# Performance work log

Measured on AMD Instinct MI355X. Metric: run time of the kernel, lower is better.

Reference implementation:

```python
import jax, jax.numpy as jnp
import numpy as np

IN_FEATURES = 2048
OUT_FEATURES = 2048
BLOCK_SIZE = 16
F_BLOCKS = (OUT_FEATURES + BLOCK_SIZE - 1) // BLOCK_SIZE  # 128
G_BLOCKS = (IN_FEATURES + BLOCK_SIZE - 1) // BLOCK_SIZE   # 128
BATCH = 4096


def setup_inputs() -> dict:
    key = jax.random.key(0)
    k1, k2, k3 = jax.random.split(key, 3)
    x = jax.random.normal(k1, (BATCH, IN_FEATURES), dtype=jnp.float32)
    # Xavier-uniform-ish scale for index vectors viewed as (f*g, block_size)
    limit = np.sqrt(6.0 / (F_BLOCKS * G_BLOCKS + BLOCK_SIZE)).astype(np.float32)
    index_vectors = jax.random.uniform(
        k2, (F_BLOCKS, G_BLOCKS, BLOCK_SIZE), dtype=jnp.float32,
        minval=-limit, maxval=limit)
    b = jax.random.normal(k3, (OUT_FEATURES,), dtype=jnp.float32) * 0.02
    return {"x": x, "index_vectors": index_vectors, "b": b}


def reference(x, index_vectors, b):
    batch = x.shape[0]
    padded_in = G_BLOCKS * BLOCK_SIZE
    padded_out = F_BLOCKS * BLOCK_SIZE
    if x.shape[1] < padded_in:
        x = jnp.pad(x, ((0, 0), (0, padded_in - x.shape[1])))
    x_blocks = x.reshape(batch, G_BLOCKS, BLOCK_SIZE)            # (B, g, b)
    # Batched FFT over all blocks at once (replaces the f*g python loop)
    fft_p = jnp.fft.fft(index_vectors, axis=-1)                  # (f, g, b) complex
    fft_x = jnp.fft.fft(x_blocks, axis=-1)                       # (B, g, b) complex
    # sum_j IFFT(P_ij * X_j) == IFFT(sum_j P_ij * X_j) by linearity of IFFT
    out_fft = jnp.einsum('fgb,Bgb->Bfb', fft_p, fft_x)           # (B, f, b) complex
    out_blocks = jnp.fft.ifft(out_fft, axis=-1).real             # (B, f, b)
    out = out_blocks.reshape(batch, padded_out)
    if padded_out > OUT_FEATURES:
        out = out[:, :OUT_FEATURES]
    return out + b
```

## Files before the change

kernel.cpp:

```cpp
#include <hip/hip_runtime.h>
#include <hip/hip_bf16.h>


#define M_DIM 4096
#define N_DIM 2048
#define K_DIM 2048
#define BK 64
#define NT (K_DIM / BK)
#define BUFSZ 49152

typedef __attribute__((ext_vector_type(8))) short bf16x8;
typedef __attribute__((ext_vector_type(4))) float f32x4;

typedef const __attribute__((address_space(1))) void gvoid_t;
typedef __attribute__((address_space(3))) void lvoid_t;

#define FENCE asm volatile("" ::: "memory")
#define BAR()  do { FENCE; __builtin_amdgcn_s_barrier(); FENCE; } while (0)
#define GLD(src, dst) __builtin_amdgcn_global_load_lds((gvoid_t*)(src), (lvoid_t*)(dst), 16, 0, 0)

#define STAGE_A(dst, src) (GLD((src) + 0 * 64 * K_DIM, (dst) + 0),     \
                           GLD((src) + 1 * 64 * K_DIM, (dst) + 8192),  \
                           GLD((src) + 2 * 64 * K_DIM, (dst) + 16384), \
                           GLD((src) + 3 * 64 * K_DIM, (dst) + 24576))
#define STAGE_B(dst, src) (GLD((src) + 0 * 64 * K_DIM, (dst) + 0),     \
                           GLD((src) + 1 * 64 * K_DIM, (dst) + 8192))

__device__ __forceinline__ unsigned int f2bf(float f) {
  unsigned int u = __float_as_uint(f);
  return (u + 0x7fffu + ((u >> 16) & 1u)) >> 16;
}

__global__ __launch_bounds__(256) void prep_kernel(const float* __restrict__ x,
                                                   const float* __restrict__ iv,
                                                   unsigned short* __restrict__ xb,
                                                   unsigned short* __restrict__ W) {
  int b = blockIdx.x;
  if (b < (M_DIM * K_DIM / 8) / 256) {
    int idx = b * 256 + threadIdx.x;
    const float4* x4 = (const float4*)x;
    float4 a = x4[idx * 2 + 0];
    float4 c = x4[idx * 2 + 1];
    uint4 o;
    o.x = f2bf(a.x) | (f2bf(a.y) << 16);
    o.y = f2bf(a.z) | (f2bf(a.w) << 16);
    o.z = f2bf(c.x) | (f2bf(c.y) << 16);
    o.w = f2bf(c.z) | (f2bf(c.w) << 16);
    ((uint4*)xb)[idx] = o;
  } else {
    int idx = (b - (M_DIM * K_DIM / 8) / 256) * 256 + threadIdx.x;
    int o  = idx >> 8;
    int i0 = (idx & 255) * 8;
    int f = o >> 4, t = o & 15;
    int g = i0 >> 4, u0 = i0 & 15;
    const float* row = iv + (f * 128 + g) * 16;
    unsigned int p[4];
#pragma unroll
    for (int j = 0; j < 4; ++j) {
      unsigned int lo = f2bf(row[(t - (u0 + 2 * j + 0)) & 15]);
      unsigned int hi = f2bf(row[(t - (u0 + 2 * j + 1)) & 15]);
      p[j] = lo | (hi << 16);
    }
    ((uint4*)W)[idx] = make_uint4(p[0], p[1], p[2], p[3]);
  }
}

__global__ __launch_bounds__(512, 2) void gemm_bias_kernel(const unsigned short* __restrict__ A,
                                                           const unsigned short* __restrict__ B,
                                                           const float* __restrict__ bias,
                                                           float* __restrict__ C) {
  __shared__ char lds[3 * BUFSZ];

  const int tid = threadIdx.x;
  const int l   = tid & 63;
  const int w   = tid >> 6;
  const int wm  = w >> 1;
  const int wn  = w & 1;

  const int orig = blockIdx.x;
  const int swz  = (orig & 7) * 32 + (orig >> 3);
  const int bm   = swz >> 4;
  const int bn   = swz & 15;

  f32x4 acc[4][4] = {};

  const int srow  = w * 8 + (l >> 3);
  const int sslot = (l & 7) ^ ((l >> 3) & 7);
  const unsigned short* Asrc0 = A + (size_t)(bm * 256 + srow) * K_DIM + sslot * 8;
  const unsigned short* Bsrc0 = B + (size_t)(bn * 128 + srow) * K_DIM + sslot * 8;

  const int fr = l & 15;
  const int rxor = (l & 7) << 4;
  const int aRow0 = (wm * 64 + fr) * 128;
  const int bRow0 = (wn * 64 + fr) * 128;
  const int swzcol0 = (0 * 64 + (l >> 4) * 16) ^ rxor;
  const int swzcol1 = (1 * 64 + (l >> 4) * 16) ^ rxor;

  bf16x8 fa[4], fb[4];

#define LDA(BUF, SWZ)                                                   \
  do {                                                                  \
    const char* Ab_ = lds + (BUF) * BUFSZ;                              \
    const char* Bb_ = Ab_ + 32768;                                      \
    _Pragma("unroll")                                                   \
    for (int m = 0; m < 4; ++m)                                         \
      fa[m] = *(const bf16x8*)(Ab_ + aRow0 + m * 2048 + (SWZ));         \
    _Pragma("unroll")                                                   \
    for (int n = 0; n < 4; ++n)                                         \
      fb[n] = *(const bf16x8*)(Bb_ + bRow0 + n * 2048 + (SWZ));         \
  } while (0)

#define MFMA_CLUSTER()                                                  \
  do {                                                                  \
    asm volatile("s_waitcnt lgkmcnt(0)" ::: "memory");                  \
    __builtin_amdgcn_sched_barrier(0);                                  \
    __builtin_amdgcn_s_setprio(1);                                      \
    _Pragma("unroll")                                                   \
    for (int m = 0; m < 4; ++m)                                         \
      _Pragma("unroll")                                                 \
      for (int n = 0; n < 4; ++n)                                       \
        acc[m][n] = __builtin_amdgcn_mfma_f32_16x16x32_bf16(fa[m], fb[n], acc[m][n], 0, 0, 0); \
    __builtin_amdgcn_s_setprio(0);                                      \
    __builtin_amdgcn_sched_barrier(0);                                  \
  } while (0)

#define PHASE(BUF, SWZ, STAGE_STMT, VM_STMT)                            \
  do {                                                                  \
    LDA(BUF, SWZ);                                                      \
    STAGE_STMT;                                                         \
    VM_STMT;                                                            \
    BAR();                                                              \
    MFMA_CLUSTER();                                                     \
    BAR();                                                              \
  } while (0)

#define VM6 asm volatile("s_waitcnt vmcnt(6)" ::: "memory")
#define VM0 asm volatile("s_waitcnt vmcnt(0)" ::: "memory")
#define NOSTAGE (void)0
#define NOVM (void)0

#define BODY(T, CUR, STG)                                               \
  do {                                                                  \
    PHASE(CUR, swzcol0, STAGE_A(lds + (STG) * BUFSZ + w * 1024, Asrc0 + ((T) + 2) * BK), NOVM); \
    PHASE(CUR, swzcol1, STAGE_B(lds + (STG) * BUFSZ + 32768 + w * 1024, Bsrc0 + ((T) + 2) * BK), VM6); \
  } while (0)

  STAGE_A(lds + 0 * BUFSZ + w * 1024, Asrc0 + 0 * BK);
  STAGE_B(lds + 0 * BUFSZ + 32768 + w * 1024, Bsrc0 + 0 * BK);
  STAGE_A(lds + 1 * BUFSZ + w * 1024, Asrc0 + 1 * BK);
  STAGE_B(lds + 1 * BUFSZ + 32768 + w * 1024, Bsrc0 + 1 * BK);
  asm volatile("s_waitcnt vmcnt(6)" ::: "memory");
  BAR();

  for (int t = 0; t < NT - 2; t += 3) {
    BODY(t + 0, 0, 2);
    BODY(t + 1, 1, 0);
    BODY(t + 2, 2, 1);
  }

  PHASE(0, swzcol0, NOSTAGE, NOVM);
  PHASE(0, swzcol1, NOSTAGE, VM0);
  LDA(1, swzcol0);
  MFMA_CLUSTER();
  LDA(1, swzcol1);
  MFMA_CLUSTER();

  const int row0 = bm * 256 + wm * 64 + (l >> 4) * 4;
  const int col0 = bn * 128 + wn * 64 + (l & 15);
#pragma unroll
  for (int n = 0; n < 4; ++n) {
    float bv = bias[col0 + n * 16];
#pragma unroll
    for (int m = 0; m < 4; ++m) {
#pragma unroll
      for (int j = 0; j < 4; ++j) {
        C[(size_t)(row0 + m * 16 + j) * N_DIM + (col0 + n * 16)] = acc[m][n][j] + bv;
      }
    }
  }
#undef BODY
#undef PHASE
#undef MFMA_CLUSTER
#undef LDA
#undef VM6
#undef VM0
#undef NOSTAGE
#undef NOVM
}

__global__ __launch_bounds__(256) void fallback_kernel(const float* __restrict__ x,
                                                       const float* __restrict__ iv,
                                                       const float* __restrict__ b,
                                                       float* __restrict__ out) {
  int idx = blockIdx.x * 256 + threadIdx.x;
  int Bn = idx >> 11, o = idx & 2047;
  int f = o >> 4, t = o & 15;
  const float* xr = x + (size_t)Bn * 2048;
  float acc = 0.f;
  for (int g = 0; g < 128; ++g) {
    const float* pr = iv + (f * 128 + g) * 16;
    const float* xg = xr + g * 16;
#pragma unroll
    for (int s = 0; s < 16; ++s) acc += pr[s] * xg[(t - s) & 15];
  }
  out[idx] = acc + b[o];
}

extern "C" void kernel_launch(void* const* d_in, const int* in_sizes, int n_in,
                              void* d_out, int out_size, void* d_ws, size_t ws_size,
                              hipStream_t stream) {
  const float* x    = (const float*)d_in[0];
  const float* iv   = (const float*)d_in[1];
  const float* bias = (const float*)d_in[2];
  float* out = (float*)d_out;

  const size_t xb_bytes = (size_t)M_DIM * K_DIM * 2;
  const size_t w_bytes  = (size_t)N_DIM * K_DIM * 2;
  if (ws_size < xb_bytes + w_bytes) {
    fallback_kernel<<<(M_DIM * N_DIM) / 256, 256, 0, stream>>>(x, iv, bias, out);
    return;
  }

  unsigned short* xb = (unsigned short*)d_ws;
  unsigned short* W  = xb + (size_t)M_DIM * K_DIM;

  const int cvt_blocks = (M_DIM * K_DIM / 8) / 256;
  const int bw_blocks  = (N_DIM * K_DIM / 8) / 256;
  prep_kernel<<<cvt_blocks + bw_blocks, 256, 0, stream>>>(x, iv, xb, W);

  gemm_bias_kernel<<<(M_DIM / 256) * (N_DIM / 128), 512, 0, stream>>>(xb, W, bias, out);
}
```

Before: 56.81 us.

## Shrink GEMM tile to 128x128 with 256 threads and double buffering

Changes the GEMM block tile from 256x128 with 8 waves to 128x128 with 4 waves, doubling the grid to 512 blocks. The three-stage LDS ring with split A/B phases becomes a two-buffer scheme: each step issues the next tile's A and B loads together, runs both MFMA clusters with a single barrier, then waits on vmcnt(0). The aim is less LDS per block, more blocks per CU and fewer barriers. The cost is lower operand reuse per block, more global traffic, and less prefetch depth, since each iteration now waits for all loads to finish.

```diff
diff --git a/kernel.cpp b/kernel.cpp
--- a/kernel.cpp
+++ b/kernel.cpp
@@ -7,7 +7,7 @@
 #define K_DIM 2048
 #define BK 64
 #define NT (K_DIM / BK)
-#define BUFSZ 49152
+#define BUFSZ 32768
 
 typedef __attribute__((ext_vector_type(8))) short bf16x8;
 typedef __attribute__((ext_vector_type(4))) float f32x4;
@@ -18,13 +18,6 @@
 #define FENCE asm volatile("" ::: "memory")
 #define BAR()  do { FENCE; __builtin_amdgcn_s_barrier(); FENCE; } while (0)
 #define GLD(src, dst) __builtin_amdgcn_global_load_lds((gvoid_t*)(src), (lvoid_t*)(dst), 16, 0, 0)
-
-#define STAGE_A(dst, src) (GLD((src) + 0 * 64 * K_DIM, (dst) + 0),     \
-                           GLD((src) + 1 * 64 * K_DIM, (dst) + 8192),  \
-                           GLD((src) + 2 * 64 * K_DIM, (dst) + 16384), \
-                           GLD((src) + 3 * 64 * K_DIM, (dst) + 24576))
-#define STAGE_B(dst, src) (GLD((src) + 0 * 64 * K_DIM, (dst) + 0),     \
-                           GLD((src) + 1 * 64 * K_DIM, (dst) + 8192))
 
 __device__ __forceinline__ unsigned int f2bf(float f) {
   unsigned int u = __float_as_uint(f);
@@ -65,11 +58,11 @@
   }
 }
 
-__global__ __launch_bounds__(512, 2) void gemm_bias_kernel(const unsigned short* __restrict__ A,
+__global__ __launch_bounds__(256, 2) void gemm_bias_kernel(const unsigned short* __restrict__ A,
                                                            const unsigned short* __restrict__ B,
                                                            const float* __restrict__ bias,
                                                            float* __restrict__ C) {
-  __shared__ char lds[3 * BUFSZ];
+  __shared__ char lds[2 * BUFSZ];
 
   const int tid = threadIdx.x;
   const int l   = tid & 63;
@@ -78,7 +71,7 @@
   const int wn  = w & 1;
 
   const int orig = blockIdx.x;
-  const int swz  = (orig & 7) * 32 + (orig >> 3);
+  const int swz  = (orig & 7) * 64 + (orig >> 3);
   const int bm   = swz >> 4;
   const int bn   = swz & 15;
 
@@ -86,7 +79,7 @@
 
   const int srow  = w * 8 + (l >> 3);
   const int sslot = (l & 7) ^ ((l >> 3) & 7);
-  const unsigned short* Asrc0 = A + (size_t)(bm * 256 + srow) * K_DIM + sslot * 8;
+  const unsigned short* Asrc0 = A + (size_t)(bm * 128 + srow) * K_DIM + sslot * 8;
   const unsigned short* Bsrc0 = B + (size_t)(bn * 128 + srow) * K_DIM + sslot * 8;
 
   const int fr = l & 15;
@@ -98,10 +91,26 @@
 
   bf16x8 fa[4], fb[4];
 
+#define STAGE_AB(BUFC, T)                                               \
+  do {                                                                  \
+    char* ad_ = lds + (BUFC) * BUFSZ + w * 1024;                        \
+    char* bd_ = ad_ + 16384;                                            \
+    const unsigned short* as_ = Asrc0 + (T) * BK;                       \
+    const unsigned short* bs_ = Bsrc0 + (T) * BK;                       \
+    GLD(as_ + 0 * 32 * K_DIM, ad_ + 0);                                 \
+    GLD(as_ + 1 * 32 * K_DIM, ad_ + 4096);                              \
+    GLD(as_ + 2 * 32 * K_DIM, ad_ + 8192);                              \
+    GLD(as_ + 3 * 32 * K_DIM, ad_ + 12288);                             \
+    GLD(bs_ + 0 * 32 * K_DIM, bd_ + 0);                                 \
+    GLD(bs_ + 1 * 32 * K_DIM, bd_ + 4096);                              \
+    GLD(bs_ + 2 * 32 * K_DIM, bd_ + 8192);                              \
+    GLD(bs_ + 3 * 32 * K_DIM, bd_ + 12288);                             \
+  } while (0)
+
 #define LDA(BUF, SWZ)                                                   \
   do {                                                                  \
     const char* Ab_ = lds + (BUF) * BUFSZ;                              \
-    const char* Bb_ = Ab_ + 32768;                                      \
+    const char* Bb_ = Ab_ + 16384;                                      \
     _Pragma("unroll")                                                   \
     for (int m = 0; m < 4; ++m)                                         \
       fa[m] = *(const bf16x8*)(Ab_ + aRow0 + m * 2048 + (SWZ));         \
@@ -124,48 +133,32 @@
     __builtin_amdgcn_sched_barrier(0);                                  \
   } while (0)
 
-#define PHASE(BUF, SWZ, STAGE_STMT, VM_STMT)                            \
-  do {                                                                  \
-    LDA(BUF, SWZ);                                                      \
-    STAGE_STMT;                                                         \
-    VM_STMT;                                                            \
+#define BODY(T, CUR, OTH)                                               \
+  do {                                                                  \
+    LDA(CUR, swzcol0);                                                  \
+    STAGE_AB(OTH, (T) + 1);                                             \
+    MFMA_CLUSTER();                                                     \
+    LDA(CUR, swzcol1);                                                  \
+    MFMA_CLUSTER();                                                     \
+    asm volatile("s_waitcnt vmcnt(0)" ::: "memory");                    \
     BAR();                                                              \
-    MFMA_CLUSTER();                                                     \
-    BAR();                                                              \
-  } while (0)
-
-#define VM6 asm volatile("s_waitcnt vmcnt(6)" ::: "memory")
-#define VM0 asm volatile("s_waitcnt vmcnt(0)" ::: "memory")
-#define NOSTAGE (void)0
-#define NOVM (void)0
-
-#define BODY(T, CUR, STG)                                               \
-  do {                                                                  \
-    PHASE(CUR, swzcol0, STAGE_A(lds + (STG) * BUFSZ + w * 1024, Asrc0 + ((T) + 2) * BK), NOVM); \
-    PHASE(CUR, swzcol1, STAGE_B(lds + (STG) * BUFSZ + 32768 + w * 1024, Bsrc0 + ((T) + 2) * BK), VM6); \
-  } while (0)
-
-  STAGE_A(lds + 0 * BUFSZ + w * 1024, Asrc0 + 0 * BK);
-  STAGE_B(lds + 0 * BUFSZ + 32768 + w * 1024, Bsrc0 + 0 * BK);
-  STAGE_A(lds + 1 * BUFSZ + w * 1024, Asrc0 + 1 * BK);
-  STAGE_B(lds + 1 * BUFSZ + 32768 + w * 1024, Bsrc0 + 1 * BK);
-  asm volatile("s_waitcnt vmcnt(6)" ::: "memory");
+  } while (0)
+
+  STAGE_AB(0, 0);
+  asm volatile("s_waitcnt vmcnt(0)" ::: "memory");
   BAR();
 
-  for (int t = 0; t < NT - 2; t += 3) {
-    BODY(t + 0, 0, 2);
+  for (int t = 0; t < NT - 2; t += 2) {
+    BODY(t + 0, 0, 1);
     BODY(t + 1, 1, 0);
-    BODY(t + 2, 2, 1);
-  }
-
-  PHASE(0, swzcol0, NOSTAGE, NOVM);
-  PHASE(0, swzcol1, NOSTAGE, VM0);
+  }
+  BODY(30, 0, 1);
   LDA(1, swzcol0);
   MFMA_CLUSTER();
   LDA(1, swzcol1);
   MFMA_CLUSTER();
 
-  const int row0 = bm * 256 + wm * 64 + (l >> 4) * 4;
+  const int row0 = bm * 128 + wm * 64 + (l >> 4) * 4;
   const int col0 = bn * 128 + wn * 64 + (l & 15);
 #pragma unroll
   for (int n = 0; n < 4; ++n) {
@@ -179,13 +172,9 @@
     }
   }
 #undef BODY
-#undef PHASE
 #undef MFMA_CLUSTER
 #undef LDA
-#undef VM6
-#undef VM0
-#undef NOSTAGE
-#undef NOVM
+#undef STAGE_AB
 }
 
 __global__ __launch_bounds__(256) void fallback_kernel(const float* __restrict__ x,
@@ -228,5 +217,5 @@
   const int bw_blocks  = (N_DIM * K_DIM / 8) / 256;
   prep_kernel<<<cvt_blocks + bw_blocks, 256, 0, stream>>>(x, iv, xb, W);
 
-  gemm_bias_kernel<<<(M_DIM / 256) * (N_DIM / 128), 512, 0, stream>>>(xb, W, bias, out);
-}
+  gemm_bias_kernel<<<(M_DIM / 128) * (N_DIM / 128), 256, 0, stream>>>(xb, W, bias, out);
+}
```

Result: no change. 57.56 us (+1.3%).
